# Optimization experiments

Hardware: AMD Instinct MI355X
Metric: run time of the kernel (lower is better)

Reference implementation:

```python
import jax, jax.numpy as jnp
import numpy as np

B, S, HID = 2, 2048, 2048
H, HKV, D = 16, 8, 128
CHUNK = 512
THETA = 1000000.0
NEG = -1e9


def setup_inputs() -> dict:
    key = jax.random.key(0)
    ks = jax.random.split(key, 10)
    hidden_states = jax.random.normal(ks[0], (B, S, HID), dtype=jnp.float32)
    # additive causal mask (0 on/below diagonal, -1e9 above)
    tri = jnp.tril(jnp.ones((S, S), dtype=bool))
    attention_mask = jnp.where(tri, 0.0, NEG).astype(jnp.float32)
    attention_mask = jnp.broadcast_to(attention_mask[None, None], (B, 1, S, S))
    w = 0.02
    Wq = jax.random.normal(ks[1], (HID, H * D), dtype=jnp.float32) * w
    bq = jax.random.normal(ks[2], (H * D,), dtype=jnp.float32) * w
    Wk = jax.random.normal(ks[3], (HID, HKV * D), dtype=jnp.float32) * w
    bk = jax.random.normal(ks[4], (HKV * D,), dtype=jnp.float32) * w
    Wv = jax.random.normal(ks[5], (HID, HKV * D), dtype=jnp.float32) * w
    bv = jax.random.normal(ks[6], (HKV * D,), dtype=jnp.float32) * w
    Wo = jax.random.normal(ks[7], (H * D, HID), dtype=jnp.float32) * w
    bo = jax.random.normal(ks[8], (HID,), dtype=jnp.float32) * w
    return {"hidden_states": hidden_states, "attention_mask": attention_mask,
            "Wq": Wq, "bq": bq, "Wk": Wk, "bk": bk, "Wv": Wv, "bv": bv,
            "Wo": Wo, "bo": bo}


def _rope_tables(seq_len, dim):
    inv_freq = 1.0 / (THETA ** (jnp.arange(0, dim, 2, dtype=jnp.float32) / dim))
    pos = jnp.arange(seq_len, dtype=jnp.float32)
    freqs = pos[:, None] * inv_freq[None, :]          # [S, D/2]
    emb = jnp.concatenate([freqs, freqs], axis=-1)    # [S, D]
    return jnp.cos(emb)[None, None], jnp.sin(emb)[None, None]  # [1,1,S,D]


def _rotate_half(x):
    x1, x2 = jnp.split(x, 2, axis=-1)
    return jnp.concatenate([-x2, x1], axis=-1)


def _attn_forward(hidden_states, attention_mask, Wq, bq, Wk, bk, Wv, bv, Wo, bo):
    bsz, s, _ = hidden_states.shape
    q = (hidden_states @ Wq + bq).reshape(bsz, s, H, D).transpose(0, 2, 1, 3)
    k = (hidden_states @ Wk + bk).reshape(bsz, s, HKV, D).transpose(0, 2, 1, 3)
    v = (hidden_states @ Wv + bv).reshape(bsz, s, HKV, D).transpose(0, 2, 1, 3)
    cos, sin = _rope_tables(s, D)
    q = q * cos + _rotate_half(q) * sin
    k = k * cos + _rotate_half(k) * sin
    n_rep = H // HKV
    k = jnp.repeat(k, n_rep, axis=1)  # repeat_kv
    v = jnp.repeat(v, n_rep, axis=1)
    scale = 1.0 / jnp.sqrt(jnp.float32(D))
    nq, nk = s // CHUNK, s // CHUNK
    Qc = q.reshape(bsz, H, nq, CHUNK, D)
    Kc = jnp.moveaxis(k.reshape(bsz, H, nk, CHUNK, D), 2, 0)   # [nk,B,H,Ck,D]
    Vc = jnp.moveaxis(v.reshape(bsz, H, nk, CHUNK, D), 2, 0)
    Mc = jnp.moveaxis(attention_mask.reshape(bsz, 1, nq, CHUNK, nk, CHUNK), 4, 0)  # [nk,B,1,nq,Cq,Ck]

    def step(carry, xs):
        o, m, d = carry
        k_seg, v_seg, m_seg = xs
        # scores: [B,H,nq,Cq,Ck]
        sc = jnp.einsum('bhqcd,bhkd->bhqck', Qc, k_seg) * scale + m_seg
        new_m = jnp.maximum(m, sc.max(axis=-1, keepdims=True))
        e = jnp.exp(sc - new_m)
        sums = e.sum(axis=-1, keepdims=True)
        prev = jnp.exp(m - new_m)          # NOTE: uses running max, as in source
        d_new = prev + sums
        o = (o * prev + jnp.einsum('bhqck,bhkd->bhqcd', e, v_seg)) / d_new
        return (o, new_m, d_new), None

    o0 = jnp.zeros((bsz, H, nq, CHUNK, D), dtype=jnp.float32)
    m0 = jnp.full((bsz, H, nq, CHUNK, 1), -jnp.inf, dtype=jnp.float32)
    d0 = jnp.ones((bsz, H, nq, CHUNK, 1), dtype=jnp.float32)
    (o, m, d), _ = jax.lax.scan(step, (o0, m0, d0), (Kc, Vc, Mc))
    # final rescale: attn_output * exp(max - logsumexp) == o / d_last (source math)
    o = o / d
    attn = o.reshape(bsz, H, s, D).transpose(0, 2, 1, 3).reshape(bsz, s, H * D)
    return attn @ Wo + bo


def reference(hidden_states, attention_mask, Wq, bq, Wk, bk, Wv, bv, Wo, bo):
    return _attn_forward(hidden_states, attention_mask, Wq, bq, Wk, bk, Wv, bv, Wo, bo)
```

## Files before the change

### kernel.cpp

```cpp
#include <hip/hip_runtime.h>
#include <hip/hip_bf16.h>


typedef __attribute__((ext_vector_type(8))) short s8v;
typedef __attribute__((ext_vector_type(4))) float f4v;
typedef __attribute__((ext_vector_type(4))) unsigned int u32x4;

#define MFMA16(a, b, c) __builtin_amdgcn_mfma_f32_16x16x32_bf16((a), (b), (c), 0, 0, 0)

typedef unsigned short u16;
typedef const __attribute__((address_space(1))) unsigned int* gas_p;
typedef __attribute__((address_space(3))) unsigned int* las_p;

template <bool B> struct BoolC { static constexpr bool value = B; };

__device__ __forceinline__ void gl_lds16(const void* g, void* l) {
    __builtin_amdgcn_global_load_lds((gas_p)g, (las_p)l, 16, 0, 0);
}

__device__ __forceinline__ u16 f2b(float f) {
    __hip_bfloat16 h = __float2bfloat16(f);
    return *reinterpret_cast<u16*>(&h);
}
__device__ __forceinline__ float b2f(u16 u) {
    __hip_bfloat16 h;
    *reinterpret_cast<u16*>(&h) = u;
    return __bfloat162float(h);
}

__device__ __forceinline__ void qswap(unsigned int& a, unsigned int& b) {
#if __has_builtin(__builtin_amdgcn_permlane32_swap) && __has_builtin(__builtin_amdgcn_permlane16_swap)
    typedef __attribute__((ext_vector_type(2))) unsigned int u32x2;
    u32x2 r1 = __builtin_amdgcn_permlane32_swap(a, b, false, false);
    u32x2 r2 = __builtin_amdgcn_permlane16_swap(r1[0], r1[1], false, false);
    a = r2[0]; b = r2[1];
#else
    asm volatile("v_permlane32_swap_b32 %0, %1\n\t"
                 "s_nop 0\n\t"
                 "v_permlane16_swap_b32 %0, %1\n\t"
                 "s_nop 0"
                 : "+v"(a), "+v"(b));
#endif
}

__device__ const unsigned char qt_tab[40] = {
    4, 5, 6, 7,
    8, 8, 9, 9, 10, 10, 11, 11,
    12, 12, 12, 13, 13, 13, 14, 14, 14, 15, 15, 15,
    3, 7, 11, 15, 2, 6, 10, 14, 1, 5, 9, 13, 0, 4, 8, 12};
__device__ const unsigned char c_tab[40] = {
    0, 0, 0, 0,
    0, 1, 0, 1, 0, 1, 0, 1,
    0, 1, 2, 0, 1, 2, 0, 1, 2, 0, 1, 2,
    0, 1, 2, 3, 0, 1, 2, 3, 0, 1, 2, 3, 0, 1, 2, 3};

__device__ __forceinline__ int uoff40(int qt, int c) {
    int qc = qt >> 2;
    if (c < qc) {
        if (qt < 8) return qt - 4;
        if (qt < 12) return 4 + ((qt - 8) << 1) + c;
        return 12 + (qt - 12) * 3 + c;
    }
    return 24 + ((3 - (qt & 3)) << 2) + qc;
}

__global__ __launch_bounds__(256) void k_cast_hs(const float* __restrict__ src,
                                                 u16* __restrict__ dst) {
    int i = blockIdx.x * 256 + threadIdx.x;
    float4 v = reinterpret_cast<const float4*>(src)[i];
    alignas(8) u16 t[4] = {f2b(v.x), f2b(v.y), f2b(v.z), f2b(v.w)};
    reinterpret_cast<uint2*>(dst)[i] = *reinterpret_cast<uint2*>(t);
}

__global__ __launch_bounds__(256) void k_transpose_w(
    const float* __restrict__ Wq, const float* __restrict__ Wk,
    const float* __restrict__ Wv, const float* __restrict__ Wo,
    u16* __restrict__ wt_all, u16* __restrict__ wo_t) {
    int id = blockIdx.x;
    const float* W; u16* dst; int N, nbase;
    if (id < 4096)      { W = Wq; dst = wt_all; N = 2048; nbase = 0; }
    else if (id < 6144) { W = Wk; dst = wt_all; N = 1024; nbase = 2048; id -= 4096; }
    else if (id < 8192) { W = Wv; dst = wt_all; N = 1024; nbase = 3072; id -= 6144; }
    else                { W = Wo; dst = wo_t;  N = 2048; nbase = 0;    id -= 8192; }
    int tiles_n = N >> 5;
    int k0 = (id / tiles_n) << 5, n0 = (id % tiles_n) << 5;
    __shared__ float t[32][33];
    int tid = threadIdx.x;
    {
        int row = tid >> 3, c4 = (tid & 7) << 2;
        float4 v = *reinterpret_cast<const float4*>(&W[(size_t)(k0 + row) * N + n0 + c4]);
        t[row][c4 + 0] = v.x; t[row][c4 + 1] = v.y;
        t[row][c4 + 2] = v.z; t[row][c4 + 3] = v.w;
    }
    __syncthreads();
    {
        int n = tid >> 3, kq = (tid & 7) << 2;
        alignas(8) u16 p[4];
#pragma unroll
        for (int j = 0; j < 4; j++) p[j] = f2b(t[kq + j][n]);
        *reinterpret_cast<uint2*>(&dst[(size_t)(nbase + n0 + n) * 2048 + k0 + kq]) =
            *reinterpret_cast<uint2*>(p);
    }
}

__global__ __launch_bounds__(256) void k_bias(const float* __restrict__ bq,
                                              const float* __restrict__ bk,
                                              const float* __restrict__ bv,
                                              float* __restrict__ dst) {
    int i = blockIdx.x * 256 + threadIdx.x;
    float v = (i < 2048) ? bq[i] : (i < 3072) ? bk[i - 2048] : bv[i - 3072];
    dst[i] = v;
}

__global__ __launch_bounds__(256) void k_gemm(
    const u16* __restrict__ A, const u16* __restrict__ Bt,
    const float* __restrict__ bias, void* __restrict__ out,
    int M, int N, int K, int out_f32) {
    __shared__ alignas(16) u16 As[128][64];
    __shared__ alignas(16) u16 Bs[128][64];
    int tid = threadIdx.x;
    int wave = tid >> 6, lane = tid & 63, quad = lane >> 4, l16 = lane & 15;
    int m0 = blockIdx.y << 7, n0 = blockIdx.x << 7;
    int wm = (wave >> 1) << 6, wn = (wave & 1) << 6;
    f4v zero = {0.f, 0.f, 0.f, 0.f};
    f4v acc[4][4];
#pragma unroll
    for (int a = 0; a < 4; a++)
#pragma unroll
        for (int b = 0; b < 4; b++) acc[a][b] = zero;
    int r0 = tid >> 3;
    int gsw = (tid & 7) ^ (r0 & 7);
    const u16* gA = A + (size_t)(m0 + r0) * K + (gsw << 3);
    const u16* gB = Bt + (size_t)(n0 + r0) * K + (gsw << 3);
    for (int k0 = 0; k0 < K; k0 += 64) {
        __syncthreads();
#pragma unroll
        for (int i = 0; i < 4; i++) {
            gl_lds16(gA + (size_t)(i << 5) * K + k0, (char*)As + (i << 12) + tid * 16);
            gl_lds16(gB + (size_t)(i << 5) * K + k0, (char*)Bs + (i << 12) + tid * 16);
        }
        __syncthreads();
#pragma unroll
        for (int ks = 0; ks < 2; ks++) {
            int rg = (((ks << 2) | quad) ^ (l16 & 7)) << 3;
            s8v af[4], bf_[4];
#pragma unroll
            for (int mi = 0; mi < 4; mi++)
                af[mi] = *reinterpret_cast<const s8v*>(&As[wm + mi * 16 + l16][rg]);
#pragma unroll
            for (int ni = 0; ni < 4; ni++)
                bf_[ni] = *reinterpret_cast<const s8v*>(&Bs[wn + ni * 16 + l16][rg]);
#pragma unroll
            for (int mi = 0; mi < 4; mi++)
#pragma unroll
                for (int ni = 0; ni < 4; ni++)
                    acc[mi][ni] = MFMA16(af[mi], bf_[ni], acc[mi][ni]);
        }
    }
#pragma unroll
    for (int mi = 0; mi < 4; mi++) {
#pragma unroll
        for (int ni = 0; ni < 4; ni++) {
            int n = n0 + wn + ni * 16 + l16;
            float bsv = bias[n];
#pragma unroll
            for (int r = 0; r < 4; r++) {
                int m = m0 + wm + mi * 16 + (quad << 2) + r;
                float v = acc[mi][ni][r] + bsv;
                if (out_f32)
                    reinterpret_cast<float*>(out)[(size_t)m * N + n] = v;
                else
                    reinterpret_cast<u16*>(out)[(size_t)m * N + n] = f2b(v);
            }
        }
    }
}

__global__ __launch_bounds__(256) void k_rope(const u16* __restrict__ qkv,
                                              u16* __restrict__ qr,
                                              u16* __restrict__ kr) {
    const float qscale = 0.08838834764831845f * 1.44269504088896340f;
    int row = blockIdx.x;
    int b = row >> 11, s = row & 2047;
    const u16* src = qkv + (size_t)row * 4096;
    __shared__ float lcs[64], lsn[64];
    int tid = threadIdx.x;
    if (tid < 64) {
        float fr = (float)s * exp2f((float)tid * -0.31143075889569023f);
        lcs[tid] = cosf(fr);
        lsn[tid] = sinf(fr);
    }
    __syncthreads();
    for (int u = tid; u < 1536; u += 256) {
        int hh, i;
        const u16* sp;
        u16* dp;
        float sc;
        if (u < 1024) {
            hh = u >> 6; i = u & 63;
            sp = src + hh * 128;
            dp = qr + ((size_t)(b * 16 + hh) * 2048 + s) * 128;
            sc = qscale;
        } else {
            int u2 = u - 1024;
            hh = u2 >> 6; i = u2 & 63;
            sp = src + 2048 + hh * 128;
            dp = kr + ((size_t)(b * 8 + hh) * 2048 + s) * 128;
            sc = 1.f;
        }
        float x1 = b2f(sp[i]);
        float x2 = b2f(sp[i + 64]);
        float cs = lcs[i], sn = lsn[i];
        dp[i]      = f2b((x1 * cs - x2 * sn) * sc);
        dp[i + 64] = f2b((x2 * cs + x1 * sn) * sc);
    }
}

__global__ __launch_bounds__(256) void k_vtrans(const u16* __restrict__ qkv,
                                                u16* __restrict__ vt) {
    int bkv = blockIdx.z, b = bkv >> 3, kv = bkv & 7;
    int s0 = blockIdx.x << 6, d0 = blockIdx.y << 5;
    __shared__ alignas(16) u16 t[32][72];
    int tid = threadIdx.x, c = tid & 31, rr = tid >> 5;
#pragma unroll
    for (int i = 0; i < 8; i++) {
        int s = s0 + rr + i * 8;
        t[c][rr + i * 8] = qkv[(size_t)(b * 2048 + s) * 4096 + 3072 + kv * 128 + d0 + c];
    }
    __syncthreads();
    int dd = tid >> 3, sc8 = (tid & 7) << 3;
    *reinterpret_cast<uint4*>(&vt[((size_t)(b * 8 + kv) * 128 + d0 + dd) * 2048 + s0 + sc8]) =
        *reinterpret_cast<const uint4*>(&t[dd][sc8]);
}

__global__ __launch_bounds__(256, 3) void k_attn_part(const u16* __restrict__ qr,
                                                      const u16* __restrict__ kr,
                                                      const u16* __restrict__ vt,
                                                      u16* __restrict__ PVp,
                                                      float* __restrict__ scp) {
    const float NINF = -__builtin_inff();
    __shared__ alignas(16) u16 Ks[2][64 * 128];
    __shared__ alignas(16) u16 Vs[128 * 64];

    int tid = threadIdx.x;
    int wv = tid >> 6, lane = tid & 63, quad = lane >> 4, l16 = lane & 15;
    int x = blockIdx.x, h = blockIdx.y, b = blockIdx.z, kvh = h >> 1;
    int qt = qt_tab[x], c = c_tab[x], qc = qt >> 2;
    bool diag = (c == qc);
    int m3 = qt & 3;
    int nt = diag ? ((m3 + 1) << 1) : 8;
    int kbase = c << 9;
    const u16* Qp = qr + ((size_t)(b * 16 + h) * 2048 + qt * 128 + wv * 32) * 128;
    const u16* Kp = kr + ((size_t)(b * 8 + kvh) * 2048) * 128;
    const u16* Vp = vt + ((size_t)(b * 8 + kvh) * 128) * 2048;

    s8v qf0[4], qf1[4];
#pragma unroll
    for (int sl = 0; sl < 4; sl++) {
        qf0[sl] = *reinterpret_cast<const s8v*>(&Qp[l16 * 128 + sl * 32 + (quad << 3)]);
        qf1[sl] = *reinterpret_cast<const s8v*>(&Qp[(16 + l16) * 128 + sl * 32 + (quad << 3)]);
    }
    s8v ones;
#pragma unroll
    for (int i = 0; i < 8; i++) ones[i] = (short)0x3F80;
    s8v pzero;
#pragma unroll
    for (int i = 0; i < 8; i++) pzero[i] = (short)0;

    int krow = tid >> 4, kg = (tid & 15) ^ krow;
    int vd = tid >> 3, vg = (tid & 7) ^ (vd & 7);
    auto stageK = [&](int t) {
        int kbt = kbase + (t << 6);
        const u16* kgp = Kp + (size_t)(kbt + krow) * 128 + (kg << 3);
        char* kd = (char*)&Ks[t & 1][0];
#pragma unroll
        for (int i = 0; i < 4; i++)
            gl_lds16(kgp + (size_t)(i << 4) * 128, kd + (i << 12) + tid * 16);
    };
    auto stageV = [&](int t) {
        int kbt = kbase + (t << 6);
        const u16* vgp = Vp + (size_t)vd * 2048 + kbt + (vg << 3);
        char* vdst = (char*)&Vs[0];
#pragma unroll
        for (int i = 0; i < 4; i++)
            gl_lds16(vgp + (size_t)(i << 5) * 2048, vdst + (i << 12) + tid * 16);
    };

    auto pack = [&](const f4v& s, bool tri, bool act, float& tmx,
                    unsigned int& wlo, unsigned int& whi) {
        if (!act) { wlo = 0u; whi = 0u; return; }
        float e[4];
#pragma unroll
        for (int r = 0; r < 4; r++) {
            float v = s[r];
            if (tri && ((quad << 2) + r > l16)) v = NINF;
            tmx = fmaxf(tmx, v);
            e[r] = __builtin_amdgcn_exp2f(v);
        }
        wlo = (unsigned int)f2b(e[0]) | ((unsigned int)f2b(e[1]) << 16);
        whi = (unsigned int)f2b(e[2]) | ((unsigned int)f2b(e[3]) << 16);
    };

    f4v zero = {0.f, 0.f, 0.f, 0.f};
    f4v u0[8], u1[8], sums0 = zero, sums1 = zero;
#pragma unroll
    for (int ni = 0; ni < 8; ni++) { u0[ni] = zero; u1[ni] = zero; }
    float tmx0 = NINF, tmx1 = NINF;
    int qg0 = wv << 1, qg1 = (wv << 1) + 1;

    auto run = [&](auto diagc) {
        constexpr bool DIAG = decltype(diagc)::value;
        stageK(0);
        for (int t = 0; t < nt; t++) {
            __syncthreads();
            stageV(t);
            if (t + 1 < nt) stageK(t + 1);
            const char* Kbuf = (const char*)&Ks[t & 1][0];
            int kgb = DIAG ? ((t << 2) - (m3 << 3)) : 0;
            s8v pa0s[2], pa1s[2];
            bool act0[2], act1[2];
#pragma unroll
            for (int s2 = 0; s2 < 2; s2++) {
                int kgA = kgb + (s2 << 1), kgB = kgA + 1;
                bool skip = DIAG && (kgA > qg1);
                bool a0 = !DIAG || (kgA <= qg0);
                bool b0 = !DIAG || (kgB <= qg0);
                bool b1 = !DIAG || (kgB <= qg1);
                act1[s2] = !skip;
                act0[s2] = !skip && a0;
                if (skip) { pa0s[s2] = pzero; pa1s[s2] = pzero; continue; }
                f4v sA0 = zero, sA1 = zero, sB0 = zero, sB1 = zero;
#pragma unroll
                for (int sl = 0; sl < 4; sl++) {
                    s8v kf = *reinterpret_cast<const s8v*>(
                        Kbuf + (((s2 << 1) << 4) + l16) * 256 +
                        ((((sl << 2) + quad) ^ l16) << 4));
                    if (a0) sA0 = MFMA16(kf, qf0[sl], sA0);
                    sA1 = MFMA16(kf, qf1[sl], sA1);
                }
                if (b1) {
#pragma unroll
                    for (int sl = 0; sl < 4; sl++) {
                        s8v kf = *reinterpret_cast<const s8v*>(
                            Kbuf + ((((s2 << 1) | 1) << 4) + l16) * 256 +
                            ((((sl << 2) + quad) ^ l16) << 4));
                        if (b0) sB0 = MFMA16(kf, qf0[sl], sB0);
                        sB1 = MFMA16(kf, qf1[sl], sB1);
                    }
                }
                unsigned int A0w, A1w, B0w, B1w;
                pack(sA1, DIAG && (kgA == qg1), true, tmx1, A0w, A1w);
                pack(sB1, DIAG && (kgB == qg1), b1, tmx1, B0w, B1w);
                qswap(A0w, B0w); qswap(A1w, B1w);
                u32x4 pw1 = {A0w, A1w, B0w, B1w};
                pa1s[s2] = __builtin_bit_cast(s8v, pw1);
                if (a0) {
                    unsigned int C0w, C1w, D0w, D1w;
                    pack(sA0, DIAG && (kgA == qg0), true, tmx0, C0w, C1w);
                    pack(sB0, DIAG && (kgB == qg0), b0, tmx0, D0w, D1w);
                    qswap(C0w, D0w); qswap(C1w, D1w);
                    u32x4 pw0 = {C0w, C1w, D0w, D1w};
                    pa0s[s2] = __builtin_bit_cast(s8v, pw0);
                } else {
                    pa0s[s2] = pa1s[s2];
                }
            }
            __syncthreads();
#pragma unroll
            for (int s2 = 0; s2 < 2; s2++) {
                if (DIAG && !act1[s2]) continue;
                bool a0 = !DIAG || act0[s2];
                if (a0) sums0 = MFMA16(pa0s[s2], ones, sums0);
                sums1 = MFMA16(pa1s[s2], ones, sums1);
#pragma unroll
                for (int ni = 0; ni < 8; ni++) {
                    s8v vf = *reinterpret_cast<const s8v*>(
                        (const char*)&Vs[0] + ((ni << 4) + l16) * 128 +
                        ((((s2 << 2) + quad) ^ (l16 & 7)) << 4));
                    if (a0) u0[ni] = MFMA16(pa0s[s2], vf, u0[ni]);
                    u1[ni] = MFMA16(pa1s[s2], vf, u1[ni]);
                }
            }
        }
    };
    if (diag) run(BoolC<true>{}); else run(BoolC<false>{});

    tmx0 = fmaxf(tmx0, __shfl_xor(tmx0, 16));
    tmx0 = fmaxf(tmx0, __shfl_xor(tmx0, 32));
    tmx1 = fmaxf(tmx1, __shfl_xor(tmx1, 16));
    tmx1 = fmaxf(tmx1, __shfl_xor(tmx1, 32));
    float m0[4], m1[4], resc0[4], resc1[4];
#pragma unroll
    for (int r = 0; r < 4; r++) {
        m0[r] = __shfl(tmx0, (quad << 2) + r);
        m1[r] = __shfl(tmx1, (quad << 2) + r);
        resc0[r] = __builtin_amdgcn_exp2f(-m0[r]);
        resc1[r] = __builtin_amdgcn_exp2f(-m1[r]);
    }
    int slot = (b * 16 + h) * 40 + x;
    u16* pvdst = PVp + (size_t)slot * 16384;
    int row0 = wv * 32 + (quad << 2);
#pragma unroll
    for (int ni = 0; ni < 8; ni++)
#pragma unroll
        for (int r = 0; r < 4; r++) {
            pvdst[(row0 + r) * 128 + ni * 16 + l16] = f2b(u0[ni][r] * resc0[r]);
            pvdst[(row0 + 16 + r) * 128 + ni * 16 + l16] = f2b(u1[ni][r] * resc1[r]);
        }
    if (l16 == 0) {
        float* scd = scp + (size_t)slot * 256 + row0;
#pragma unroll
        for (int r = 0; r < 4; r++) {
            scd[r] = m0[r] * 0.6931471805599453f;
            scd[16 + r] = m1[r] * 0.6931471805599453f;
            scd[128 + r] = sums0[r] * resc0[r];
            scd[144 + r] = sums1[r] * resc1[r];
        }
    }
}

__global__ __launch_bounds__(256) void k_attn_comb(const u16* __restrict__ PVp,
                                                   const float* __restrict__ scp,
                                                   u16* __restrict__ attnb) {
    int qt64 = blockIdx.x, h = blockIdx.y, b = blockIdx.z;
    int qt = qt64 >> 1, qc = qt >> 2;
    int tid = threadIdx.x;
    int row = ((qt64 & 1) << 6) + (tid >> 2), d0 = (tid & 3) << 5;
    int bh = b * 16 + h;
    float o[32];
#pragma unroll
    for (int i = 0; i < 32; i++) o[i] = 0.f;
    float mprev = -__builtin_inff(), dlast = 1.f;
    for (int cc = 0; cc <= qc; cc++) {
        int slot = bh * 40 + uoff40(qt, cc);
        float ch = scp[(size_t)slot * 256 + row];
        float sh = scp[(size_t)slot * 256 + 128 + row];
        float mnew = fmaxf(mprev, ch);
        float p = __expf(mprev - mnew);
        float lam = __expf(ch - mnew);
        float dd = p + lam * sh;
        float inv = 1.f / dd;
        const u16* pv = PVp + (size_t)slot * 16384 + row * 128 + d0;
#pragma unroll
        for (int k = 0; k < 4; k++) {
            s8v v8 = *reinterpret_cast<const s8v*>(pv + (k << 3));
#pragma unroll
            for (int j = 0; j < 8; j++) {
                int i = (k << 3) + j;
                o[i] = (o[i] * p + lam * b2f((u16)v8[j])) * inv;
            }
        }
        mprev = mnew;
        dlast = dd;
    }
    if (qc == 3) {
        float inv = 1.f / dlast;
#pragma unroll
        for (int i = 0; i < 32; i++) o[i] *= inv;
    }
    alignas(16) u16 ob[32];
#pragma unroll
    for (int i = 0; i < 32; i++) ob[i] = f2b(o[i]);
    u16* dst = attnb + (size_t)(b * 2048 + qt * 128 + row) * 2048 + h * 128 + d0;
#pragma unroll
    for (int k = 0; k < 4; k++)
        reinterpret_cast<uint4*>(dst)[k] = reinterpret_cast<const uint4*>(ob)[k];
}

extern "C" void kernel_launch(void* const* d_in, const int* in_sizes, int n_in,
                              void* d_out, int out_size, void* d_ws, size_t ws_size,
                              hipStream_t stream) {
    (void)in_sizes; (void)n_in; (void)out_size; (void)ws_size;
    const float* hs = (const float*)d_in[0];
    const float* Wq = (const float*)d_in[2];
    const float* bq = (const float*)d_in[3];
    const float* Wk = (const float*)d_in[4];
    const float* bk = (const float*)d_in[5];
    const float* Wv = (const float*)d_in[6];
    const float* bv = (const float*)d_in[7];
    const float* Wo = (const float*)d_in[8];
    const float* bo = (const float*)d_in[9];

    char* ws = (char*)d_ws;
    u16* hsb      = (u16*)(ws);
    u16* qr       = hsb;
    u16* attnb    = hsb;
    u16* wt_all   = (u16*)(ws + (16u << 20));
    u16* kr       = wt_all;
    u16* vt       = (u16*)(ws + (24u << 20));
    u16* wo_t     = (u16*)(ws + (32u << 20));
    float* bias_c = (float*)(ws + (40u << 20));
    u16* qkv      = (u16*)(ws + (40u << 20) + 65536);
    u16* PVp      = qkv;
    float* scp    = (float*)(ws + (40u << 20) + 65536 + 41943040u);

    k_cast_hs<<<8192, 256, 0, stream>>>(hs, hsb);
    k_transpose_w<<<12288, 256, 0, stream>>>(Wq, Wk, Wv, Wo, wt_all, wo_t);
    k_bias<<<16, 256, 0, stream>>>(bq, bk, bv, bias_c);
    k_gemm<<<dim3(32, 32), 256, 0, stream>>>(hsb, wt_all, bias_c, qkv,
                                             4096, 4096, 2048, 0);
    k_rope<<<4096, 256, 0, stream>>>(qkv, qr, kr);
    k_vtrans<<<dim3(32, 4, 16), 256, 0, stream>>>(qkv, vt);
    k_attn_part<<<dim3(40, 16, 2), 256, 0, stream>>>(qr, kr, vt, PVp, scp);
    k_attn_comb<<<dim3(32, 16, 2), 256, 0, stream>>>(PVp, scp, attnb);
    k_gemm<<<dim3(16, 32), 256, 0, stream>>>(attnb, wo_t, bo, d_out,
                                             4096, 2048, 2048, 1);
}
```

Measured before the change: 378.1 us.

## Double-buffer GEMM LDS tiles, swizzle workgroup order, stage epilogue through LDS

The GEMM now keeps two LDS buffers so the global-to-LDS load of the next K tile is issued before the MFMAs on the current tile, and it drops one barrier per iteration. Workgroup IDs are remapped into 4x4 tile groups spread round-robin across 8 slots, aimed at better L2 reuse across XCDs. The epilogue writes results into LDS and then stores full rows with 16-byte coalesced writes, replacing scattered 2- and 4-byte stores. This doubles LDS use to 64KB per block, which may reduce occupancy. The remap assumes gridDim.x is a multiple of 4 and that the grid divides evenly into the group layout.

```diff
diff --git a/kernel.cpp b/kernel.cpp
--- a/kernel.cpp
+++ b/kernel.cpp
@@ -116,11 +116,18 @@
     const u16* __restrict__ A, const u16* __restrict__ Bt,
     const float* __restrict__ bias, void* __restrict__ out,
     int M, int N, int K, int out_f32) {
-    __shared__ alignas(16) u16 As[128][64];
-    __shared__ alignas(16) u16 Bs[128][64];
+    __shared__ alignas(16) u16 As[2][128][64];
+    __shared__ alignas(16) u16 Bs[2][128][64];
     int tid = threadIdx.x;
     int wave = tid >> 6, lane = tid & 63, quad = lane >> 4, l16 = lane & 15;
-    int m0 = blockIdx.y << 7, n0 = blockIdx.x << 7;
+    int nwg = gridDim.x * gridDim.y;
+    int wg = blockIdx.y * gridDim.x + blockIdx.x;
+    int l = (wg & 7) * (nwg >> 3) + (wg >> 3);
+    int t4 = l >> 4, a4 = l & 15;
+    int tn4 = gridDim.x >> 2;
+    int tm = t4 / tn4, tn = t4 % tn4;
+    int m0 = ((tm << 2) + (a4 >> 2)) << 7;
+    int n0 = ((tn << 2) + (a4 & 3)) << 7;
     int wm = (wave >> 1) << 6, wn = (wave & 1) << 6;
     f4v zero = {0.f, 0.f, 0.f, 0.f};
     f4v acc[4][4];
@@ -132,46 +139,82 @@
     int gsw = (tid & 7) ^ (r0 & 7);
     const u16* gA = A + (size_t)(m0 + r0) * K + (gsw << 3);
     const u16* gB = Bt + (size_t)(n0 + r0) * K + (gsw << 3);
-    for (int k0 = 0; k0 < K; k0 += 64) {
-        __syncthreads();
+    auto stage = [&](int k0, int buf) {
 #pragma unroll
         for (int i = 0; i < 4; i++) {
-            gl_lds16(gA + (size_t)(i << 5) * K + k0, (char*)As + (i << 12) + tid * 16);
-            gl_lds16(gB + (size_t)(i << 5) * K + k0, (char*)Bs + (i << 12) + tid * 16);
-        }
-        __syncthreads();
+            gl_lds16(gA + (size_t)(i << 5) * K + k0,
+                     (char*)&As[buf][0][0] + (i << 12) + tid * 16);
+            gl_lds16(gB + (size_t)(i << 5) * K + k0,
+                     (char*)&Bs[buf][0][0] + (i << 12) + tid * 16);
+        }
+    };
+    int NT = K >> 6;
+    stage(0, 0);
+    __syncthreads();
+    for (int t = 0; t < NT; t++) {
+        int cur = t & 1;
+        if (t + 1 < NT) stage((t + 1) << 6, cur ^ 1);
 #pragma unroll
         for (int ks = 0; ks < 2; ks++) {
             int rg = (((ks << 2) | quad) ^ (l16 & 7)) << 3;
             s8v af[4], bf_[4];
 #pragma unroll
             for (int mi = 0; mi < 4; mi++)
-                af[mi] = *reinterpret_cast<const s8v*>(&As[wm + mi * 16 + l16][rg]);
+                af[mi] = *reinterpret_cast<const s8v*>(&As[cur][wm + mi * 16 + l16][rg]);
 #pragma unroll
             for (int ni = 0; ni < 4; ni++)
-                bf_[ni] = *reinterpret_cast<const s8v*>(&Bs[wn + ni * 16 + l16][rg]);
+                bf_[ni] = *reinterpret_cast<const s8v*>(&Bs[cur][wn + ni * 16 + l16][rg]);
 #pragma unroll
             for (int mi = 0; mi < 4; mi++)
 #pragma unroll
                 for (int ni = 0; ni < 4; ni++)
                     acc[mi][ni] = MFMA16(af[mi], bf_[ni], acc[mi][ni]);
         }
-    }
-#pragma unroll
-    for (int mi = 0; mi < 4; mi++) {
+        __syncthreads();
+    }
+    if (!out_f32) {
+        u16* cs = &As[0][0][0];
 #pragma unroll
         for (int ni = 0; ni < 4; ni++) {
-            int n = n0 + wn + ni * 16 + l16;
-            float bsv = bias[n];
-#pragma unroll
-            for (int r = 0; r < 4; r++) {
-                int m = m0 + wm + mi * 16 + (quad << 2) + r;
-                float v = acc[mi][ni][r] + bsv;
-                if (out_f32)
-                    reinterpret_cast<float*>(out)[(size_t)m * N + n] = v;
-                else
-                    reinterpret_cast<u16*>(out)[(size_t)m * N + n] = f2b(v);
+            float bsv = bias[n0 + wn + ni * 16 + l16];
+#pragma unroll
+            for (int mi = 0; mi < 4; mi++)
+#pragma unroll
+                for (int r = 0; r < 4; r++)
+                    cs[(wm + mi * 16 + (quad << 2) + r) * 128 + wn + ni * 16 + l16] =
+                        f2b(acc[mi][ni][r] + bsv);
+        }
+        __syncthreads();
+        int row = tid >> 1, c0 = (tid & 1) << 6;
+        u16* dst = (u16*)out + (size_t)(m0 + row) * N + n0 + c0;
+#pragma unroll
+        for (int j = 0; j < 8; j++)
+            *reinterpret_cast<uint4*>(dst + j * 8) =
+                *reinterpret_cast<const uint4*>(&cs[row * 128 + c0 + j * 8]);
+    } else {
+        float* cf = (float*)&As[0][0][0];
+#pragma unroll
+        for (int p = 0; p < 2; p++) {
+            __syncthreads();
+            if ((wm >> 6) == p) {
+#pragma unroll
+                for (int ni = 0; ni < 4; ni++) {
+                    float bsv = bias[n0 + wn + ni * 16 + l16];
+#pragma unroll
+                    for (int mi = 0; mi < 4; mi++)
+#pragma unroll
+                        for (int r = 0; r < 4; r++)
+                            cf[((wm - (p << 6)) + mi * 16 + (quad << 2) + r) * 128 +
+                               wn + ni * 16 + l16] = acc[mi][ni][r] + bsv;
+                }
             }
+            __syncthreads();
+            int row = tid >> 2, q4 = (tid & 3) << 5;
+            float* dst = (float*)out + (size_t)(m0 + (p << 6) + row) * N + n0 + q4;
+#pragma unroll
+            for (int j = 0; j < 8; j++)
+                *reinterpret_cast<uint4*>(dst + j * 4) =
+                    *reinterpret_cast<const uint4*>(&cf[row * 128 + q4 + j * 4]);
         }
     }
 }
```

New measurement: 364.8 us. 3.5% less time.
